# Kernel optimization log

Measured on AMD Instinct MI355X. Metric: run time of the kernel, lower is better.

The kernel has to match this reference:

```python
import math
import jax, jax.numpy as jnp
import numpy as np

D_MODEL = 1024
N_HEADS = 16
HEAD_DIM = D_MODEL // N_HEADS
ROPE_BASE = 10000.0
EPS = 1e-6


def rmsnorm(x, w, eps=EPS):
    # x: (..., head_dim); computed in fp32 like the torch code
    xf = x.astype(jnp.float32)
    rms = jax.lax.rsqrt(jnp.mean(xf * xf, axis=-1, keepdims=True) + eps)
    return (xf * rms).astype(x.dtype) * w


def apply_rope(x, cos, sin):
    # x: (B, H, T, head_dim); cos/sin: (T, head_dim/2)
    d2 = x.shape[-1] // 2
    x1, x2 = x[..., :d2], x[..., d2:]
    c = cos[None, None, :, :]
    s = sin[None, None, :, :]
    return jnp.concatenate([x1 * c - x2 * s, x2 * c + x1 * s], axis=-1)


def setup_inputs() -> dict:
    key = jax.random.key(0)
    ks = jax.random.split(key, 7)
    B, T = 2, 2048
    x = jax.random.normal(ks[0], (B, T, D_MODEL), dtype=jnp.float32)
    scale = 1.0 / math.sqrt(D_MODEL)
    Wq = jax.random.normal(ks[1], (D_MODEL, D_MODEL), dtype=jnp.float32) * scale
    Wk = jax.random.normal(ks[2], (D_MODEL, D_MODEL), dtype=jnp.float32) * scale
    Wv = jax.random.normal(ks[3], (D_MODEL, D_MODEL), dtype=jnp.float32) * scale
    Wo = jax.random.normal(ks[4], (D_MODEL, D_MODEL), dtype=jnp.float32) * scale
    q_norm_w = jnp.ones((HEAD_DIM,), dtype=jnp.float32)
    k_norm_w = jnp.ones((HEAD_DIM,), dtype=jnp.float32)
    return {"x": x, "Wq": Wq, "Wk": Wk, "Wv": Wv, "Wo": Wo,
            "q_norm_w": q_norm_w, "k_norm_w": k_norm_w}


def reference(x, Wq, Wk, Wv, Wo, q_norm_w, k_norm_w):
    B, T, d = x.shape
    H, hd = N_HEADS, HEAD_DIM
    # projections (nn.Linear applies x @ W.T; here W is stored as (in,out))
    q = (x @ Wq).reshape(B, T, H, hd).transpose(0, 2, 1, 3)  # (B,H,T,hd)
    k = (x @ Wk).reshape(B, T, H, hd).transpose(0, 2, 1, 3)
    v = (x @ Wv).reshape(B, T, H, hd).transpose(0, 2, 1, 3)
    # QK RMSNorm per head
    q = rmsnorm(q, q_norm_w)
    k = rmsnorm(k, k_norm_w)
    # rotary embeddings
    inv_freq = 1.0 / (ROPE_BASE ** (jnp.arange(0, hd, 2, dtype=jnp.float32) / hd))
    t = jnp.arange(T, dtype=jnp.float32)
    freqs = jnp.outer(t, inv_freq)  # (T, hd/2)
    cos, sin = jnp.cos(freqs), jnp.sin(freqs)
    q = apply_rope(q, cos, sin)
    k = apply_rope(k, cos, sin)
    # naive full attention with causal mask
    scale = 1.0 / math.sqrt(hd)
    attn = jnp.einsum('bhqd,bhkd->bhqk', q, k) * scale  # (B,H,T,T)
    causal = jnp.triu(jnp.full((T, T), -jnp.inf, dtype=attn.dtype), k=1)
    attn = attn + causal[None, None, :, :]
    attn = jax.nn.softmax(attn, axis=-1)
    out = jnp.einsum('bhqk,bhkd->bhqd', attn, v)
    out = out.transpose(0, 2, 1, 3).reshape(B, T, d)
    return out @ Wo
```

## Files before the change

kernel.cpp:

```cpp
#include <hip/hip_runtime.h>

typedef unsigned short u16;
typedef unsigned int   u32;
typedef __bf16 bf16x8 __attribute__((ext_vector_type(8)));
typedef float  f32x4  __attribute__((ext_vector_type(4)));
typedef float  f32x2  __attribute__((ext_vector_type(2)));
typedef u32    u32x4  __attribute__((ext_vector_type(4)));
typedef u16    u16x4  __attribute__((ext_vector_type(4)));

#define D_MODEL 1024
#define T_SEQ   2048
#define NH      16
#define HD      64

#define QSCALE  0.18033688011112042f
#define NEG8L2E -11.541560327111707f

__device__ __forceinline__ float b2f(u16 u){ return __uint_as_float(((u32)u)<<16); }
__device__ __forceinline__ u16 f2b(float f){
  u32 x = __float_as_uint(f);
  x += 0x7fffu + ((x>>16)&1u);
  return (u16)(x>>16);
}

__device__ __forceinline__ void gll16(const void* g, void* l){
  __builtin_amdgcn_global_load_lds((const __attribute__((address_space(1))) unsigned int*)g,
                                   (__attribute__((address_space(3))) unsigned int*)l, 16, 0, 0);
}

__global__ __launch_bounds__(256) void prep(
    const float* __restrict__ X, u16* __restrict__ Xb,
    const float* __restrict__ W0, const float* __restrict__ W1,
    const float* __restrict__ W2, const float* __restrict__ W3,
    u16* __restrict__ T0, u16* __restrict__ T1,
    u16* __restrict__ T2, u16* __restrict__ T3,
    float* __restrict__ cs)
{
  __shared__ u16 s[32][33];
  const int id = blockIdx.x, tid = threadIdx.x;
  if (id < 4096){
    const int i = (id*256 + tid)<<2;
    f32x4 v = *(const f32x4*)(X + i);
    u16x4 o;
    o[0]=f2b(v[0]); o[1]=f2b(v[1]); o[2]=f2b(v[2]); o[3]=f2b(v[3]);
    *(u16x4*)(Xb + i) = o;
  } else if (id < 8192){
    const int wid = id - 4096;
    const int z = wid >> 10, tile = wid & 1023;
    const float* src = (z==0)?W0:(z==1)?W1:(z==2)?W2:W3;
    u16*         dst = (z==0)?T0:(z==1)?T1:(z==2)?T2:T3;
    const int x = tid & 7, y = tid >> 3;
    const int r0 = (tile>>5)*32, c0 = (tile&31)*32;
    f32x4 v = *(const f32x4*)(src + (r0 + y)*D_MODEL + c0 + 4*x);
    #pragma unroll
    for (int k=0;k<4;k++) s[y][4*x+k] = f2b(v[k]);
    __syncthreads();
    u16x4 o;
    #pragma unroll
    for (int k=0;k<4;k++) o[k] = s[4*x+k][y];
    *(u16x4*)(dst + (c0 + y)*D_MODEL + r0 + 4*x) = o;
  } else {
    const int gid = (id-8192)*256 + tid;
    const int t = gid >> 5, fi = gid & 31;
    const float invf = expf(-(float)fi * 0.2878231366242558f);
    float sn, cn;
    sincosf((float)t * invf, &sn, &cn);
    cs[gid*2]   = cn;
    cs[gid*2+1] = sn;
  }
}

__global__ __launch_bounds__(256) void gemm_qkv(
    const u16* __restrict__ A, const u16* __restrict__ Bt,
    const float* __restrict__ qw, const float* __restrict__ kw,
    const float* __restrict__ cs,
    u16* __restrict__ Qb, u16* __restrict__ Kb, u16* __restrict__ Vt)
{
  __shared__ __align__(16) u16 sA[1024*8];
  __shared__ __align__(16) u16 sB[1024*8];
  const int id = blockIdx.x;
  const int xcd = id & 7, slot = id >> 3;
  const int bn = (xcd & 1)*12 + (slot % 12);
  const int bm = (xcd >> 1)*8 + (slot / 12);
  const int bm0 = bm<<7, bn0 = bn<<7;

  const int tid = threadIdx.x;
  const int lane = tid & 63;
  const int w  = tid>>6;
  const int wm = (w>>1)<<6;
  const int wn = (w&1)<<6;
  const int quad = lane>>4, lr = lane&15;
  const int swl = lr & 7;

  int rS[4], cS[4];
  #pragma unroll
  for (int i=0;i<4;i++){
    int s = i*256 + tid;
    rS[i] = s>>3;
    cS[i] = (s&7) ^ (rS[i]&7);
  }

  const f32x4 z4 = {0.f,0.f,0.f,0.f};
  f32x4 acc[4][4];
  #pragma unroll
  for (int i=0;i<4;i++)
    #pragma unroll
    for (int j=0;j<4;j++) acc[i][j] = z4;

  for (int kt=0; kt<D_MODEL; kt+=64){
    #pragma unroll
    for (int i=0;i<4;i++)
      gll16(A  + (bm0+rS[i])*D_MODEL + kt + cS[i]*8, sA + (i*256 + w*64)*8);
    #pragma unroll
    for (int i=0;i<4;i++)
      gll16(Bt + (bn0+rS[i])*D_MODEL + kt + cS[i]*8, sB + (i*256 + w*64)*8);
    __syncthreads();
    #pragma unroll
    for (int kk=0; kk<2; ++kk){
      bf16x8 af[4], bfr[4];
      const int cq = (kk*4 + quad) ^ swl;
      #pragma unroll
      for (int i=0;i<4;i++) af[i]  = *(const bf16x8*)(sA + ((wm + (i<<4) + lr)*8 + cq)*8);
      #pragma unroll
      for (int j=0;j<4;j++) bfr[j] = *(const bf16x8*)(sB + ((wn + (j<<4) + lr)*8 + cq)*8);
      #pragma unroll
      for (int i=0;i<4;i++)
        #pragma unroll
        for (int j=0;j<4;j++)
          acc[i][j] = __builtin_amdgcn_mfma_f32_16x16x32_bf16(af[i], bfr[j], acc[i][j], 0, 0, 0);
    }
    __syncthreads();
  }

  const int z = bn0 >> 10;
  const int ncl = bn0 & 1023;
  const int rq = quad<<2;

  if (z == 2){
    #pragma unroll
    for (int i=0;i<4;i++){
      int row0 = bm0 + wm + (i<<4) + rq;
      int bb = row0 >> 11, tt = row0 & (T_SEQ-1);
      #pragma unroll
      for (int j=0;j<4;j++){
        int nv = ncl + wn + (j<<4) + lr;
        int hh = nv >> 6, dd = nv & 63;
        u16* basep = Vt + ((bb*NH + hh)*HD + dd)*T_SEQ;
        #pragma unroll
        for (int r=0;r<4;r++){
          int t = tt + r;
          int pt = (t & ~63) + ((t&15)<<2) + ((t>>4)&3);
          basep[pt] = f2b(acc[i][j][r]);
        }
      }
    }
  } else {
    const float* w_ = (z==0) ? qw : kw;
    u16* dst = (z==0) ? Qb : Kb;
    const float scale = (z==0) ? QSCALE : 1.0f;
    float wv[4];
    #pragma unroll
    for (int j=0;j<4;j++) wv[j] = w_[(j<<4) + lr];
    #pragma unroll
    for (int i=0;i<4;i++){
      #pragma unroll
      for (int r=0;r<4;r++){
        const int grow = bm0 + wm + (i<<4) + rq + r;
        float ss = 0.f;
        #pragma unroll
        for (int j=0;j<4;j++) ss += acc[i][j][r]*acc[i][j][r];
        #pragma unroll
        for (int off=8; off>=1; off>>=1) ss += __shfl_xor(ss, off, 64);
        const float rms = rsqrtf(ss*(1.0f/64.0f) + 1e-6f);
        float xn[4];
        #pragma unroll
        for (int j=0;j<4;j++) xn[j] = acc[i][j][r]*rms*wv[j];
        const int t = grow & (T_SEQ-1);
        f32x2 c0 = *(const f32x2*)(cs + (t*32 + lr)*2);
        f32x2 c1 = *(const f32x2*)(cs + (t*32 + 16 + lr)*2);
        float o0 = xn[0]*c0[0] - xn[2]*c0[1];
        float o2 = xn[2]*c0[0] + xn[0]*c0[1];
        float o1 = xn[1]*c1[0] - xn[3]*c1[1];
        float o3 = xn[3]*c1[0] + xn[1]*c1[1];
        u16* rp = dst + grow*D_MODEL + ncl + wn + lr;
        rp[0]  = f2b(o0*scale);
        rp[16] = f2b(o1*scale);
        rp[32] = f2b(o2*scale);
        rp[48] = f2b(o3*scale);
      }
    }
  }
}

__global__ __launch_bounds__(256) void gemm_out(
    const u16* __restrict__ A, const u16* __restrict__ Bt, float* __restrict__ out)
{
  __shared__ __align__(16) u16 sA[256*8];
  __shared__ __align__(16) u16 sB[1024*8];
  const int id = blockIdx.x;
  const int xcd = id & 7, slot = id >> 3;
  const int bm = xcd*16 + (slot>>3);
  const int bn = slot & 7;
  const int bm0 = bm<<5, bn0 = bn<<7;

  const int tid = threadIdx.x;
  const int lane = tid & 63;
  const int w  = tid>>6;
  const int wm = (w>>1)<<4;
  const int wn = (w&1)<<6;
  const int quad = lane>>4, lr = lane&15;
  const int swl = lr & 7;

  const int rA = tid>>3, cA = (tid&7) ^ (rA&7);
  int rB[4], cB[4];
  #pragma unroll
  for (int i=0;i<4;i++){
    int s = i*256 + tid;
    rB[i] = s>>3;
    cB[i] = (s&7) ^ (rB[i]&7);
  }

  const f32x4 z4 = {0.f,0.f,0.f,0.f};
  f32x4 acc[4];
  #pragma unroll
  for (int j=0;j<4;j++) acc[j] = z4;

  for (int kt=0; kt<D_MODEL; kt+=64){
    gll16(A + (bm0+rA)*D_MODEL + kt + cA*8, sA + (w*64)*8);
    #pragma unroll
    for (int i=0;i<4;i++)
      gll16(Bt + (bn0+rB[i])*D_MODEL + kt + cB[i]*8, sB + (i*256 + w*64)*8);
    __syncthreads();
    #pragma unroll
    for (int kk=0; kk<2; ++kk){
      const int cq = (kk*4 + quad) ^ swl;
      bf16x8 af = *(const bf16x8*)(sA + ((wm + lr)*8 + cq)*8);
      #pragma unroll
      for (int j=0;j<4;j++){
        bf16x8 bfr = *(const bf16x8*)(sB + ((wn + (j<<4) + lr)*8 + cq)*8);
        acc[j] = __builtin_amdgcn_mfma_f32_16x16x32_bf16(af, bfr, acc[j], 0, 0, 0);
      }
    }
    __syncthreads();
  }

  const int rq = quad<<2;
  #pragma unroll
  for (int r=0;r<4;r++){
    const int grow = bm0 + wm + rq + r;
    #pragma unroll
    for (int j=0;j<4;j++)
      out[grow*D_MODEL + bn0 + wn + (j<<4) + lr] = acc[j][r];
  }
}

__global__ __launch_bounds__(256) void attn_mfma(const u16* __restrict__ Qb, const u16* __restrict__ Kb,
                                                 const u16* __restrict__ Vt, u16* __restrict__ AO)
{
  __shared__ __align__(16) u16 sK [2][4096];
  __shared__ __align__(16) u16 sV [4096];
  __shared__ __align__(16) u16 sP [4][1024];
  const int tid = threadIdx.x;
  const int h  = blockIdx.x, b = blockIdx.y;
  const int qt = 31 - blockIdx.z;
  const int w = tid>>6, lane = tid&63;
  const int quad = lane>>4, lr = lane&15;
  const int q8 = quad<<3;

  const int s0 = w*64 + lane, s1 = 256 + w*64 + lane;
  const int r0s = s0>>3, c0s = (s0&7)^(r0s&7);
  const int r1s = s1>>3, c1s = (s1&7)^(r1s&7);
  const u16* Kbase = Kb + (b*T_SEQ)*D_MODEL + h*HD;
  const u16* Vbase = Vt + (b*NH + h)*HD*T_SEQ;
  const int ldsOff0 = (w*64)*8, ldsOff1 = (256 + w*64)*8;

  const u16* Qrow = Qb + (b*T_SEQ + qt*64 + w*16 + lr)*D_MODEL + h*HD;
  bf16x8 qf0 = *(const bf16x8*)(Qrow + q8);
  bf16x8 qf1 = *(const bf16x8*)(Qrow + 32 + q8);

  f32x4 o[4];
  float lp[4];
  const f32x4 z4 = {0.f,0.f,0.f,0.f};
  const f32x4 ci = {NEG8L2E, NEG8L2E, NEG8L2E, NEG8L2E};
  #pragma unroll
  for (int r=0;r<4;r++) lp[r] = 0.f;
  #pragma unroll
  for (int nt=0;nt<4;nt++) o[nt] = z4;

  u16* myP = sP[w];

  gll16(Kbase + r0s*D_MODEL + c0s*8, &sK[0][ldsOff0]);
  gll16(Kbase + r1s*D_MODEL + c1s*8, &sK[0][ldsOff1]);
  __syncthreads();

  for (int kt=0; kt<=qt; ++kt){
    const int cur = kt&1;
    if (kt < qt){
      const int kn = kt+1, nb = cur^1;
      gll16(Kbase + (kn*64 + r0s)*D_MODEL + c0s*8, &sK[nb][ldsOff0]);
      gll16(Kbase + (kn*64 + r1s)*D_MODEL + c1s*8, &sK[nb][ldsOff1]);
    }
    gll16(Vbase + r0s*T_SEQ + kt*64 + c0s*8, &sV[ldsOff0]);
    gll16(Vbase + r1s*T_SEQ + kt*64 + c1s*8, &sV[ldsOff1]);

    f32x4 s4[4];
    #pragma unroll
    for (int ct=0; ct<4; ++ct){
      const int row = ct*16 + lr;
      const int sw = row&7;
      bf16x8 k0 = *(const bf16x8*)(&sK[cur][(row*8 + (quad     ^ sw))*8]);
      bf16x8 k1 = *(const bf16x8*)(&sK[cur][(row*8 + ((4+quad) ^ sw))*8]);
      f32x4 acc = ci;
      acc = __builtin_amdgcn_mfma_f32_16x16x32_bf16(qf0, k0, acc, 0,0,0);
      acc = __builtin_amdgcn_mfma_f32_16x16x32_bf16(qf1, k1, acc, 0,0,0);
      s4[ct] = acc;
    }

    if (kt == qt){
      #pragma unroll
      for (int ct=0; ct<4; ++ct){
        int col = ct*16 + lr;
        #pragma unroll
        for (int r=0;r<4;r++)
          if (col > w*16 + quad*4 + r) s4[ct][r] = -1e30f;
      }
    }

    #pragma unroll
    for (int r=0;r<4;r++){
      u16x4 pk;
      #pragma unroll
      for (int ct=0; ct<4; ++ct){
        float p = exp2f(s4[ct][r]);
        u32 pu = __float_as_uint(p) & 0xffff0000u;
        lp[r] += __uint_as_float(pu);
        pk[ct] = (u16)(pu>>16);
      }
      const int prow = quad*4 + r;
      const int pidx = prow*64 + (((lr>>1) ^ (prow&7))<<3) + ((lr&1)<<2);
      *(u16x4*)(myP + pidx) = pk;
    }

    __syncthreads();

    #pragma unroll
    for (int st=0; st<2; ++st){
      bf16x8 pf = *(const bf16x8*)(myP + lr*64 + (((st*4+quad) ^ (lr&7))<<3));
      #pragma unroll
      for (int nt=0;nt<4;nt++){
        const int row = nt*16 + lr;
        const int slotv = row*8 + ((st*4+quad) ^ (row&7));
        bf16x8 vf = *(const bf16x8*)(&sV[slotv*8]);
        o[nt] = __builtin_amdgcn_mfma_f32_16x16x32_bf16(pf, vf, o[nt], 0,0,0);
      }
    }
    __syncthreads();
  }

  #pragma unroll
  for (int r=0;r<4;r++){
    #pragma unroll
    for (int off=8; off>=1; off>>=1) lp[r] += __shfl_xor(lp[r], off, 64);
  }
  const int rowg = b*T_SEQ + qt*64 + w*16 + quad*4;
  #pragma unroll
  for (int r=0;r<4;r++){
    float inv = 1.0f / lp[r];
    #pragma unroll
    for (int nt=0;nt<4;nt++)
      AO[(rowg + r)*D_MODEL + h*HD + nt*16 + lr] = f2b(o[nt][r]*inv);
  }
}

extern "C" void kernel_launch(void* const* d_in, const int* in_sizes, int n_in,
                              void* d_out, int out_size, void* d_ws, size_t ws_size,
                              hipStream_t stream)
{
  const float* X  = (const float*)d_in[0];
  const float* Wq = (const float*)d_in[1];
  const float* Wk = (const float*)d_in[2];
  const float* Wv = (const float*)d_in[3];
  const float* Wo = (const float*)d_in[4];
  const float* qw = (const float*)d_in[5];
  const float* kw = (const float*)d_in[6];

  char* ws = (char*)d_ws;
  const size_t MB = 1024*1024;
  u16*   WqkvT = (u16*)(ws + 0*MB);
  u16*   WoT   = (u16*)(ws + 6*MB);
  u16*   Xb    = (u16*)(ws + 8*MB);
  u16*   Qb    = (u16*)(ws + 16*MB);
  u16*   Kb    = (u16*)(ws + 24*MB);
  u16*   Vt    = (u16*)(ws + 32*MB);
  u16*   AO    = (u16*)(ws + 40*MB);
  float* CS    = (float*)(ws + 48*MB);

  prep<<<dim3(8448), 256, 0, stream>>>(X, Xb, Wq, Wk, Wv, Wo,
      WqkvT, WqkvT + 1024*1024, WqkvT + 2*1024*1024, WoT, CS);
  gemm_qkv<<<dim3(768), 256, 0, stream>>>(Xb, WqkvT, qw, kw, CS, Qb, Kb, Vt);
  attn_mfma<<<dim3(NH, 2, 32), 256, 0, stream>>>(Qb, Kb, Vt, AO);
  gemm_out<<<dim3(1024), 256, 0, stream>>>(AO, WoT, (float*)d_out);
}
```

Measured before the change: 191.8 us.

## Double-buffer V tiles in attention and stage V-transpose stores through LDS

The attention kernel now prefetches the next V tile into a second LDS buffer alongside the next K tile, instead of loading V for the current tile inside the loop. It also drops the barrier between writing P and the PV MFMAs, since each wave only reads its own P buffer. In the QKV GEMM, the transposed V output is first written to a swizzled LDS scratch that reuses the operand buffers, then stored to global memory as 16-byte contiguous chunks rather than scattered 2-byte writes. The cost is an extra 8 KB of LDS per attention block, which may lower occupancy, plus an additional barrier in the GEMM epilogue.

New measurement: 187.1 us. 2.4% less time.

```diff
diff --git a/kernel.cpp b/kernel.cpp
--- a/kernel.cpp
+++ b/kernel.cpp
@@ -7,6 +7,7 @@
 typedef float  f32x2  __attribute__((ext_vector_type(2)));
 typedef u32    u32x4  __attribute__((ext_vector_type(4)));
 typedef u16    u16x4  __attribute__((ext_vector_type(4)));
+typedef u16    u16x8  __attribute__((ext_vector_type(8)));
 
 #define D_MODEL 1024
 #define T_SEQ   2048
@@ -76,8 +77,9 @@
     const float* __restrict__ cs,
     u16* __restrict__ Qb, u16* __restrict__ Kb, u16* __restrict__ Vt)
 {
-  __shared__ __align__(16) u16 sA[1024*8];
-  __shared__ __align__(16) u16 sB[1024*8];
+  __shared__ __align__(16) u16 smem[2048*8];
+  u16* sA = smem;
+  u16* sB = smem + 1024*8;
   const int id = blockIdx.x;
   const int xcd = id & 7, slot = id >> 3;
   const int bn = (xcd & 1)*12 + (slot % 12);
@@ -137,22 +139,35 @@
   const int rq = quad<<2;
 
   if (z == 2){
+    u16* sT = smem;
     #pragma unroll
     for (int i=0;i<4;i++){
-      int row0 = bm0 + wm + (i<<4) + rq;
-      int bb = row0 >> 11, tt = row0 & (T_SEQ-1);
+      const int ttb = wm + (i<<4) + rq;
       #pragma unroll
       for (int j=0;j<4;j++){
-        int nv = ncl + wn + (j<<4) + lr;
-        int hh = nv >> 6, dd = nv & 63;
-        u16* basep = Vt + ((bb*NH + hh)*HD + dd)*T_SEQ;
+        const int nv = wn + (j<<4) + lr;
+        const int sw = nv & 15;
         #pragma unroll
         for (int r=0;r<4;r++){
-          int t = tt + r;
-          int pt = (t & ~63) + ((t&15)<<2) + ((t>>4)&3);
-          basep[pt] = f2b(acc[i][j][r]);
+          const int tt = ttb + r;
+          const int ttp = ((tt&15)<<2) | ((tt>>4)&3) | (tt&64);
+          sT[(nv*16 + ((ttp>>3) ^ sw))*8 + (ttp&7)] = f2b(acc[i][j][r]);
         }
       }
+    }
+    __syncthreads();
+    const int nv = tid>>1;
+    const int bb = bm0 >> 11;
+    const int tt0 = bm0 & (T_SEQ-1);
+    const int ncol = ncl + nv;
+    const int hh = ncol >> 6, dd = ncol & 63;
+    u16* basep = Vt + ((bb*NH + hh)*HD + dd)*T_SEQ + tt0;
+    const int sw = nv & 15;
+    #pragma unroll
+    for (int cc=0; cc<8; ++cc){
+      const int g = ((tid&1)<<3) + cc;
+      u16x8 vv = *(const u16x8*)(sT + (nv*16 + (g ^ sw))*8);
+      *(u16x8*)(basep + g*8) = vv;
     }
   } else {
     const float* w_ = (z==0) ? qw : kw;
@@ -258,7 +273,7 @@
                                                  const u16* __restrict__ Vt, u16* __restrict__ AO)
 {
   __shared__ __align__(16) u16 sK [2][4096];
-  __shared__ __align__(16) u16 sV [4096];
+  __shared__ __align__(16) u16 sVT[2][4096];
   __shared__ __align__(16) u16 sP [4][1024];
   const int tid = threadIdx.x;
   const int h  = blockIdx.x, b = blockIdx.y;
@@ -291,6 +306,8 @@
 
   gll16(Kbase + r0s*D_MODEL + c0s*8, &sK[0][ldsOff0]);
   gll16(Kbase + r1s*D_MODEL + c1s*8, &sK[0][ldsOff1]);
+  gll16(Vbase + r0s*T_SEQ + c0s*8,   &sVT[0][ldsOff0]);
+  gll16(Vbase + r1s*T_SEQ + c1s*8,   &sVT[0][ldsOff1]);
   __syncthreads();
 
   for (int kt=0; kt<=qt; ++kt){
@@ -299,9 +316,9 @@
       const int kn = kt+1, nb = cur^1;
       gll16(Kbase + (kn*64 + r0s)*D_MODEL + c0s*8, &sK[nb][ldsOff0]);
       gll16(Kbase + (kn*64 + r1s)*D_MODEL + c1s*8, &sK[nb][ldsOff1]);
-    }
-    gll16(Vbase + r0s*T_SEQ + kt*64 + c0s*8, &sV[ldsOff0]);
-    gll16(Vbase + r1s*T_SEQ + kt*64 + c1s*8, &sV[ldsOff1]);
+      gll16(Vbase + r0s*T_SEQ + kn*64 + c0s*8,     &sVT[nb][ldsOff0]);
+      gll16(Vbase + r1s*T_SEQ + kn*64 + c1s*8,     &sVT[nb][ldsOff1]);
+    }
 
     f32x4 s4[4];
     #pragma unroll
@@ -341,8 +358,6 @@
       *(u16x4*)(myP + pidx) = pk;
     }
 
-    __syncthreads();
-
     #pragma unroll
     for (int st=0; st<2; ++st){
       bf16x8 pf = *(const bf16x8*)(myP + lr*64 + (((st*4+quad) ^ (lr&7))<<3));
@@ -350,7 +365,7 @@
       for (int nt=0;nt<4;nt++){
         const int row = nt*16 + lr;
         const int slotv = row*8 + ((st*4+quad) ^ (row&7));
-        bf16x8 vf = *(const bf16x8*)(&sV[slotv*8]);
+        bf16x8 vf = *(const bf16x8*)(&sVT[cur][slotv*8]);
         o[nt] = __builtin_amdgcn_mfma_f32_16x16x32_bf16(pf, vf, o[nt], 0,0,0);
       }
     }
```
